# Kernel tuning notes

Measured on AMD Instinct MI355X. Metric: run time of the kernel, lower is better.

Reference implementation:

```python
import jax, jax.numpy as jnp
import numpy as np

N_NODES = 100000
N_EDGES = 1600000
FEAT = 128
HID = 128
CLASSES = 10
GRAPHS = 64


def gcn_conv(x, W, b, src, dst, n):
    # PyG GCNConv: h = x @ W; add self-loops; symmetric deg^{-1/2} norm; scatter-add; + bias
    h = x @ W
    src_f = jnp.concatenate([src, jnp.arange(n, dtype=src.dtype)])
    dst_f = jnp.concatenate([dst, jnp.arange(n, dtype=dst.dtype)])
    deg = jax.ops.segment_sum(jnp.ones_like(dst_f, dtype=h.dtype), dst_f, num_segments=n)
    dinv = jax.lax.rsqrt(jnp.where(deg > 0, deg, 1.0))
    norm = dinv[src_f] * dinv[dst_f]              # [E+N]
    msg = h[src_f] * norm[:, None]                # gather + scale
    out = jax.ops.segment_sum(msg, dst_f, num_segments=n)  # scatter-add
    return out + b


def global_mean_pool(x, batch, num_graphs):
    s = jax.ops.segment_sum(x, batch, num_segments=num_graphs)
    cnt = jax.ops.segment_sum(jnp.ones_like(batch, dtype=x.dtype), batch, num_segments=num_graphs)
    return s / jnp.maximum(cnt, 1.0)[:, None]


def setup_inputs() -> dict:
    key = jax.random.key(0)
    ks = jax.random.split(key, 10)
    x = jax.random.normal(ks[0], (N_NODES, FEAT), dtype=jnp.float32)
    edge_index = jax.random.randint(ks[1], (2, N_EDGES), 0, N_NODES, dtype=jnp.int64)
    batch = jnp.sort(jax.random.randint(ks[2], (N_NODES,), 0, GRAPHS, dtype=jnp.int64))
    def glorot(k, fi, fo):
        s = float(np.sqrt(6.0 / (fi + fo)))
        return jax.random.uniform(k, (fi, fo), jnp.float32, -s, s)
    return {
        "x": x, "edge_index": edge_index, "batch": batch,
        "W1": glorot(ks[3], FEAT, HID), "b1": jnp.zeros((HID,), jnp.float32),
        "W2": glorot(ks[4], HID, HID), "b2": jnp.zeros((HID,), jnp.float32),
        "W3": glorot(ks[5], HID, HID), "b3": jnp.zeros((HID,), jnp.float32),
        "Wlin": glorot(ks[6], HID, CLASSES), "blin": jnp.zeros((CLASSES,), jnp.float32),
    }


def reference(x, edge_index, batch, W1, b1, W2, b2, W3, b3, Wlin, blin):
    src, dst = edge_index[0], edge_index[1]
    n = x.shape[0]
    h = jax.nn.relu(gcn_conv(x, W1, b1, src, dst, n))
    h = jax.nn.relu(gcn_conv(h, W2, b2, src, dst, n))
    h = gcn_conv(h, W3, b3, src, dst, n)
    emb = global_mean_pool(h, batch, GRAPHS)      # [GRAPHS, HID]
    # dropout(p=0.5) is identity in eval mode
    logits = emb @ Wlin + blin                    # [GRAPHS, CLASSES]
    return logits, jnp.squeeze(emb)
```

## Files before the change

kernel.cpp:

```cpp
#include <hip/hip_runtime.h>
#include <hip/hip_bf16.h>
#include <stdint.h>

typedef unsigned int uint32;
typedef __attribute__((ext_vector_type(8))) short short8;
typedef __attribute__((ext_vector_type(4))) float float4v;

#define FEAT 128
#define NGRAPH 64
#define SBLK 256
#define STHR 256
#define SSEG 2
#define GB   256
#define NBK  512

__device__ __forceinline__ float bf2f_lo(uint32 v) {
    union { uint32 i; float f; } u; u.i = v << 16; return u.f;
}
__device__ __forceinline__ float bf2f_hi(uint32 v) {
    union { uint32 i; float f; } u; u.i = v & 0xffff0000u; return u.f;
}
__device__ __forceinline__ unsigned short f2bf(float f) {
    uint32 u = __builtin_bit_cast(uint32, f);
    uint32 r = (u + 0x7fffu + ((u >> 16) & 1u)) >> 16;
    return (unsigned short)r;
}
__device__ __forceinline__ uint32 f2bf2(float lo, float hi) {
    return (uint32)f2bf(lo) | ((uint32)f2bf(hi) << 16);
}

__global__ void k_bhist(const int* __restrict__ dst, int* __restrict__ bhist, int E) {
    __shared__ int h[NBK];
    int t = threadIdx.x, blk = blockIdx.x;
    for (int b = t; b < NBK; b += 256) h[b] = 0;
    __syncthreads();
    int chunk = (E + GB - 1) / GB;
    int lo = blk * chunk, hi = min(lo + chunk, E);
    for (int e = lo + t; e < hi; e += 256)
        atomicAdd(&h[dst[e] >> 8], 1);
    __syncthreads();
    for (int b = t; b < NBK; b += 256) bhist[blk * NBK + b] = h[b];
}

__global__ void k_boffs(int* __restrict__ bhist, int* __restrict__ bbase) {
    __shared__ int sc[NBK];
    int t = threadIdx.x;
    int tot = 0;
    for (int blk = 0; blk < GB; blk++) {
        int v = bhist[blk * NBK + t];
        bhist[blk * NBK + t] = tot;
        tot += v;
    }
    sc[t] = tot;
    __syncthreads();
    for (int off = 1; off < NBK; off <<= 1) {
        int v = (t >= off) ? sc[t - off] : 0;
        __syncthreads();
        sc[t] += v;
        __syncthreads();
    }
    bbase[t] = sc[t] - tot;
    if (t == NBK - 1) bbase[NBK] = sc[t];
}

__global__ void k_bscat(const int* __restrict__ src, const int* __restrict__ dst,
                        const int* __restrict__ bhist, const int* __restrict__ bbase,
                        uint32* __restrict__ ebuf, int E) {
    __shared__ int cur[NBK];
    int t = threadIdx.x, blk = blockIdx.x;
    for (int b = t; b < NBK; b += 256) cur[b] = bbase[b] + bhist[blk * NBK + b];
    __syncthreads();
    int chunk = (E + GB - 1) / GB;
    int lo = blk * chunk, hi = min(lo + chunk, E);
    for (int e = lo + t; e < hi; e += 256) {
        int d = dst[e], s = src[e];
        int b = d >> 8;
        int p = atomicAdd(&cur[b], 1);
        ebuf[p] = ((uint32)s << 8) | (uint32)(d & 255);
    }
}

__global__ void k_count2(const uint32* __restrict__ ebuf, const int* __restrict__ bbase,
                         int* __restrict__ counts, float* __restrict__ dinv, int N) {
    __shared__ int h[256];
    int t = threadIdx.x, b = blockIdx.x;
    h[t] = 0;
    __syncthreads();
    int e0 = bbase[b], e1 = bbase[b + 1];
    for (int e = e0 + t; e < e1; e += 256)
        atomicAdd(&h[ebuf[e] & 255u], 1);
    __syncthreads();
    int node = b * 256 + t;
    if (node < N) {
        counts[node] = h[t];
        dinv[node] = rsqrtf((float)h[t] + 1.0f);
    }
}

__global__ void k_fill2(const uint32* __restrict__ ebuf, const int* __restrict__ bbase,
                        const int* __restrict__ rowp, int* __restrict__ csrc, int N) {
    __shared__ int cur[256];
    int t = threadIdx.x, b = blockIdx.x;
    int node = b * 256 + t;
    cur[t] = (node < N) ? rowp[node] : 0;
    __syncthreads();
    int e0 = bbase[b], e1 = bbase[b + 1];
    for (int e = e0 + t; e < e1; e += 256) {
        uint32 v = ebuf[e];
        int p = atomicAdd(&cur[v & 255u], 1);
        csrc[p] = (int)(v >> 8);
    }
}

__global__ void k_scan_a(const int* __restrict__ counts, int* __restrict__ tbase,
                         int* __restrict__ bsum, int N) {
    __shared__ int sc[STHR];
    int t = threadIdx.x, b = blockIdx.x;
    int g = b * STHR + t;
    int lo = g * SSEG;
    int s = 0;
#pragma unroll
    for (int j = 0; j < SSEG; j++) {
        int i = lo + j;
        if (i < N) s += counts[i];
    }
    sc[t] = s;
    __syncthreads();
    for (int off = 1; off < STHR; off <<= 1) {
        int v = (t >= off) ? sc[t - off] : 0;
        __syncthreads();
        sc[t] += v;
        __syncthreads();
    }
    tbase[g] = sc[t] - s;
    if (t == STHR - 1) bsum[b] = sc[t];
}

__global__ void k_scan_b(const int* __restrict__ bsum, int* __restrict__ bbase2,
                         int* __restrict__ rowp, int N) {
    __shared__ int sc[SBLK];
    int t = threadIdx.x;
    int s = bsum[t];
    sc[t] = s;
    __syncthreads();
    for (int off = 1; off < SBLK; off <<= 1) {
        int v = (t >= off) ? sc[t - off] : 0;
        __syncthreads();
        sc[t] += v;
        __syncthreads();
    }
    bbase2[t] = sc[t] - s;
    if (t == SBLK - 1) rowp[N] = sc[t];
}

__global__ void k_scan_c(const int* __restrict__ counts, const int* __restrict__ tbase,
                         const int* __restrict__ bbase2, int* __restrict__ rowp, int N) {
    int t = threadIdx.x, b = blockIdx.x;
    int g = b * STHR + t;
    int base = bbase2[b] + tbase[g];
    int lo = g * SSEG;
#pragma unroll
    for (int j = 0; j < SSEG; j++) {
        int i = lo + j;
        if (i < N) { rowp[i] = base; base += counts[i]; }
    }
}

__global__ void k_wswz3(const float* __restrict__ W1, const float* __restrict__ W2,
                        const float* __restrict__ W3, unsigned short* __restrict__ o1,
                        unsigned short* __restrict__ o2, unsigned short* __restrict__ o3) {
    int wid = blockIdx.x >> 3;
    const float* W = (wid == 0) ? W1 : (wid == 1) ? W2 : W3;
    unsigned short* out = (wid == 0) ? o1 : (wid == 1) ? o2 : o3;
    int e = (blockIdx.x & 7) * 256 + threadIdx.x;
    int kt = e >> 9, ct = (e >> 6) & 7, lane = e & 63;
    int krow = kt * 32 + (lane >> 4) * 8;
    int col = ct * 16 + (lane & 15);
#pragma unroll
    for (int j = 0; j < 8; j++)
        out[e * 8 + j] = f2bf(W[(krow + j) * FEAT + col]);
}

template <bool F32IN>
__global__ void k_gemm(const void* __restrict__ Xp,
                       const unsigned short* __restrict__ Wswz,
                       const float* __restrict__ dinv,
                       unsigned short* __restrict__ Hb, int N) {
    __shared__ unsigned short Wl[FEAT * FEAT];
    {
        const uint4* Wg = (const uint4*)Wswz;
        uint4* Ws = (uint4*)Wl;
        for (int i = threadIdx.x; i < 2048; i += 256) Ws[i] = Wg[i];
    }
    __syncthreads();

    int wave = threadIdx.x >> 6, lane = threadIdx.x & 63;
    int r0 = (blockIdx.x * 4 + wave) * 16;
    if (r0 >= N) return;
    int m = lane & 15, q = lane >> 4;

    int arow = r0 + m; if (arow >= N) arow = N - 1;
    short8 a[4];
    if (F32IN) {
        const float* Ar = (const float*)Xp + (long)arow * FEAT;
#pragma unroll
        for (int kt = 0; kt < 4; kt++) {
            float4 u = *(const float4*)(Ar + kt * 32 + q * 8);
            float4 v = *(const float4*)(Ar + kt * 32 + q * 8 + 4);
            short8 t;
            t[0] = (short)f2bf(u.x); t[1] = (short)f2bf(u.y);
            t[2] = (short)f2bf(u.z); t[3] = (short)f2bf(u.w);
            t[4] = (short)f2bf(v.x); t[5] = (short)f2bf(v.y);
            t[6] = (short)f2bf(v.z); t[7] = (short)f2bf(v.w);
            a[kt] = t;
        }
    } else {
        const short8* Ar = (const short8*)((const unsigned short*)Xp + (long)arow * FEAT);
#pragma unroll
        for (int kt = 0; kt < 4; kt++) a[kt] = Ar[kt * 4 + q];
    }

    const short8* Bl = (const short8*)Wl;
    float4v acc[8];
#pragma unroll
    for (int ct = 0; ct < 8; ct++) acc[ct] = (float4v){0.f, 0.f, 0.f, 0.f};

#pragma unroll
    for (int ct = 0; ct < 8; ct++) {
        acc[ct] = __builtin_amdgcn_mfma_f32_16x16x32_bf16(a[0], Bl[(0 * 8 + ct) * 64 + lane], acc[ct], 0, 0, 0);
        acc[ct] = __builtin_amdgcn_mfma_f32_16x16x32_bf16(a[1], Bl[(1 * 8 + ct) * 64 + lane], acc[ct], 0, 0, 0);
        acc[ct] = __builtin_amdgcn_mfma_f32_16x16x32_bf16(a[2], Bl[(2 * 8 + ct) * 64 + lane], acc[ct], 0, 0, 0);
        acc[ct] = __builtin_amdgcn_mfma_f32_16x16x32_bf16(a[3], Bl[(3 * 8 + ct) * 64 + lane], acc[ct], 0, 0, 0);
    }

    float ds[4];
#pragma unroll
    for (int reg = 0; reg < 4; reg++) {
        int row = r0 + q * 4 + reg;
        ds[reg] = (row < N) ? dinv[row] : 0.f;
    }
#pragma unroll
    for (int ct = 0; ct < 8; ct++) {
#pragma unroll
        for (int reg = 0; reg < 4; reg++) {
            int row = r0 + q * 4 + reg;
            if (row < N) Hb[(long)row * FEAT + ct * 16 + m] = f2bf(acc[ct][reg] * ds[reg]);
        }
    }
}

__global__ void k_agg(const uint32* __restrict__ Hb,
                      const int* __restrict__ rowp, const int* __restrict__ csrc,
                      const float* __restrict__ dinv, const float* __restrict__ bias,
                      uint32* __restrict__ OUTb, int N, int relu) {
    int wave = threadIdx.x >> 6, lane = threadIdx.x & 63;
    int i = blockIdx.x * 4 + wave;
    if (i >= N) return;
    int f = lane & 31, half = lane >> 5;
    const uint2* H2 = (const uint2*)Hb;
    float a0 = 0.f, a1 = 0.f, a2 = 0.f, a3 = 0.f;
    int e0 = rowp[i], e1 = rowp[i + 1];
    int e = e0;
    for (; e + 16 <= e1; e += 16) {
        int  s[8];
        uint2 h[8];
#pragma unroll
        for (int j = 0; j < 8; j++) s[j] = csrc[e + 2 * j + half];
#pragma unroll
        for (int j = 0; j < 8; j++) h[j] = H2[(long)s[j] * 32 + f];
#pragma unroll
        for (int j = 0; j < 8; j++) {
            a0 += bf2f_lo(h[j].x); a1 += bf2f_hi(h[j].x);
            a2 += bf2f_lo(h[j].y); a3 += bf2f_hi(h[j].y);
        }
    }
    {
        int r = e1 - e;
        int  s[8];
        uint2 h[8];
#pragma unroll
        for (int j = 0; j < 8; j++) {
            int idx = 2 * j + half;
            if (idx < r) s[j] = csrc[e + idx];
        }
#pragma unroll
        for (int j = 0; j < 8; j++)
            if (2 * j + half < r) h[j] = H2[(long)s[j] * 32 + f];
#pragma unroll
        for (int j = 0; j < 8; j++)
            if (2 * j + half < r) {
                a0 += bf2f_lo(h[j].x); a1 += bf2f_hi(h[j].x);
                a2 += bf2f_lo(h[j].y); a3 += bf2f_hi(h[j].y);
            }
    }
    a0 += __shfl_xor(a0, 32);
    a1 += __shfl_xor(a1, 32);
    a2 += __shfl_xor(a2, 32);
    a3 += __shfl_xor(a3, 32);
    if (half == 0) {
        uint2 hv = H2[(long)i * 32 + f];
        a0 += bf2f_lo(hv.x); a1 += bf2f_hi(hv.x);
        a2 += bf2f_lo(hv.y); a3 += bf2f_hi(hv.y);
        float di = dinv[i];
        float4 bb = ((const float4*)bias)[f];
        a0 = a0 * di + bb.x; a1 = a1 * di + bb.y;
        a2 = a2 * di + bb.z; a3 = a3 * di + bb.w;
        if (relu) {
            a0 = fmaxf(a0, 0.f); a1 = fmaxf(a1, 0.f);
            a2 = fmaxf(a2, 0.f); a3 = fmaxf(a3, 0.f);
        }
        uint2 o;
        o.x = f2bf2(a0, a1);
        o.y = f2bf2(a2, a3);
        ((uint2*)OUTb)[(long)i * 32 + f] = o;
    }
}

__global__ void k_pool(const uint32* __restrict__ Gb, const int* __restrict__ batch,
                       float* __restrict__ pool, int* __restrict__ cntg, int N) {
    int t = threadIdx.x;
    int nb = gridDim.x;
    int chunk = (N + nb - 1) / nb;
    int lo = blockIdx.x * chunk, hi = min(lo + chunk, N);
    if (lo >= hi) return;
    float ax = 0.f, ay = 0.f;
    int cnt = 0;
    int cg = batch[lo];
    for (int i = lo; i < hi; i++) {
        int g = batch[i];
        if (g != cg) {
            atomicAdd(&pool[cg * FEAT + 2 * t], ax);
            atomicAdd(&pool[cg * FEAT + 2 * t + 1], ay);
            if (t == 0) atomicAdd(&cntg[cg], cnt);
            ax = ay = 0.f; cnt = 0; cg = g;
        }
        uint32 v = Gb[(long)i * 64 + t];
        ax += bf2f_lo(v); ay += bf2f_hi(v);
        cnt++;
    }
    atomicAdd(&pool[cg * FEAT + 2 * t], ax);
    atomicAdd(&pool[cg * FEAT + 2 * t + 1], ay);
    if (t == 0) atomicAdd(&cntg[cg], cnt);
}

__global__ void k_final(const float* __restrict__ pool, const int* __restrict__ cntg,
                        const float* __restrict__ Wlin, const float* __restrict__ blin,
                        float* __restrict__ out) {
    __shared__ float es[FEAT];
    int g = blockIdx.x, t = threadIdx.x;
    float c = (float)max(cntg[g], 1);
    float e = pool[g * FEAT + t] / c;
    es[t] = e;
    out[NGRAPH * 10 + g * FEAT + t] = e;
    __syncthreads();
    if (t < 10) {
        float a = blin[t];
        for (int k = 0; k < FEAT; k++)
            a += es[k] * Wlin[k * 10 + t];
        out[g * 10 + t] = a;
    }
}

extern "C" void kernel_launch(void* const* d_in, const int* in_sizes, int n_in,
                              void* d_out, int out_size, void* d_ws, size_t ws_size,
                              hipStream_t stream) {
    const float* x    = (const float*)d_in[0];
    const int*   ei   = (const int*)d_in[1];
    const int*   batch= (const int*)d_in[2];
    const float* W1   = (const float*)d_in[3];
    const float* b1   = (const float*)d_in[4];
    const float* W2   = (const float*)d_in[5];
    const float* b2   = (const float*)d_in[6];
    const float* W3   = (const float*)d_in[7];
    const float* b3   = (const float*)d_in[8];
    const float* Wlin = (const float*)d_in[9];
    const float* blin = (const float*)d_in[10];

    const int N = in_sizes[2];
    const int E = in_sizes[1] / 2;
    const int* src = ei;
    const int* dst = ei + E;
    const int NB = (N + 255) >> 8;

    char* w = (char*)d_ws;
    auto take = [&](size_t bytes) {
        char* p = w;
        w += (bytes + 255) & ~(size_t)255;
        return p;
    };
    int*    counts = (int*)   take((size_t)N * 4);
    float*  dinv   = (float*) take((size_t)N * 4);
    int*    rowp   = (int*)   take((size_t)(N + 1) * 4);
    int*    csrc   = (int*)   take((size_t)E * 4);
    uint32* ebuf   = (uint32*)take((size_t)E * 4);
    int*    bhist  = (int*)   take((size_t)GB * NBK * 4);
    int*    bbase  = (int*)   take((size_t)(NBK + 1) * 4);
    uint32* hbuf   = (uint32*)take((size_t)N * FEAT * 2);
    uint32* gbuf   = (uint32*)take((size_t)N * FEAT * 2);
    unsigned short* w1s = (unsigned short*)take(FEAT * FEAT * 2);
    unsigned short* w2s = (unsigned short*)take(FEAT * FEAT * 2);
    unsigned short* w3s = (unsigned short*)take(FEAT * FEAT * 2);
    float*  pool   = (float*) take((size_t)NGRAPH * FEAT * 4);
    int*    cntg   = (int*)   take((size_t)NGRAPH * 4);
    int*    tbase  = (int*)   take((size_t)SBLK * STHR * 4);
    int*    bsum   = (int*)   take((size_t)SBLK * 4);
    int*    bbase2 = (int*)   take((size_t)SBLK * 4);
    (void)ws_size; (void)n_in; (void)out_size;

    hipMemsetAsync(pool, 0, (size_t)NGRAPH * FEAT * 4, stream);
    hipMemsetAsync(cntg, 0, (size_t)NGRAPH * 4, stream);

    k_bhist <<<GB, 256, 0, stream>>>(dst, bhist, E);
    k_boffs <<<1, NBK, 0, stream>>>(bhist, bbase);
    k_bscat <<<GB, 256, 0, stream>>>(src, dst, bhist, bbase, ebuf, E);
    k_count2<<<NB, 256, 0, stream>>>(ebuf, bbase, counts, dinv, N);
    k_scan_a<<<SBLK, STHR, 0, stream>>>(counts, tbase, bsum, N);
    k_scan_b<<<1, SBLK, 0, stream>>>(bsum, bbase2, rowp, N);
    k_scan_c<<<SBLK, STHR, 0, stream>>>(counts, tbase, bbase2, rowp, N);
    k_fill2 <<<NB, 256, 0, stream>>>(ebuf, bbase, rowp, csrc, N);

    k_wswz3<<<24, 256, 0, stream>>>(W1, W2, W3, w1s, w2s, w3s);

    const int gemm_blocks = (N + 63) / 64;
    const int agg_blocks  = (N + 3) / 4;

    k_gemm<true> <<<gemm_blocks, 256, 0, stream>>>(x, w1s, dinv, (unsigned short*)hbuf, N);
    k_agg <<<agg_blocks, 256, 0, stream>>>(hbuf, rowp, csrc, dinv, b1, gbuf, N, 1);
    k_gemm<false><<<gemm_blocks, 256, 0, stream>>>(gbuf, w2s, dinv, (unsigned short*)hbuf, N);
    k_agg <<<agg_blocks, 256, 0, stream>>>(hbuf, rowp, csrc, dinv, b2, gbuf, N, 1);
    k_gemm<false><<<gemm_blocks, 256, 0, stream>>>(gbuf, w3s, dinv, (unsigned short*)hbuf, N);
    k_agg <<<agg_blocks, 256, 0, stream>>>(hbuf, rowp, csrc, dinv, b3, gbuf, N, 0);

    k_pool <<<1024, 64, 0, stream>>>(gbuf, batch, pool, cntg, N);
    k_final<<<NGRAPH, 128, 0, stream>>>(pool, cntg, Wlin, blin, (float*)d_out);
}
```

Before: 464.7 us.

## Fuse aggregation with next-layer GEMM and merge CSR count, scan and fill

New measurement: 637.5 us. 1.37x slower.

```diff
diff --git a/kernel.cpp b/kernel.cpp
--- a/kernel.cpp
+++ b/kernel.cpp
@@ -8,9 +8,6 @@
 
 #define FEAT 128
 #define NGRAPH 64
-#define SBLK 256
-#define STHR 256
-#define SSEG 2
 #define GB   256
 #define NBK  512
 
@@ -29,7 +26,7 @@
     return (uint32)f2bf(lo) | ((uint32)f2bf(hi) << 16);
 }
 
-__global__ void k_bhist(const int* __restrict__ dst, int* __restrict__ bhist, int E) {
+__global__ void k_bhist(const int* __restrict__ dst, int* __restrict__ bhistT, int E) {
     __shared__ int h[NBK];
     int t = threadIdx.x, blk = blockIdx.x;
     for (int b = t; b < NBK; b += 256) h[b] = 0;
@@ -39,16 +36,17 @@
     for (int e = lo + t; e < hi; e += 256)
         atomicAdd(&h[dst[e] >> 8], 1);
     __syncthreads();
-    for (int b = t; b < NBK; b += 256) bhist[blk * NBK + b] = h[b];
-}
-
-__global__ void k_boffs(int* __restrict__ bhist, int* __restrict__ bbase) {
+    for (int b = t; b < NBK; b += 256) bhistT[b * GB + blk] = h[b];
+}
+
+__global__ void k_boffs(int* __restrict__ bhistT, int* __restrict__ bbase) {
     __shared__ int sc[NBK];
     int t = threadIdx.x;
     int tot = 0;
+#pragma unroll 8
     for (int blk = 0; blk < GB; blk++) {
-        int v = bhist[blk * NBK + t];
-        bhist[blk * NBK + t] = tot;
+        int v = bhistT[t * GB + blk];
+        bhistT[t * GB + blk] = tot;
         tot += v;
     }
     sc[t] = tot;
@@ -64,11 +62,11 @@
 }
 
 __global__ void k_bscat(const int* __restrict__ src, const int* __restrict__ dst,
-                        const int* __restrict__ bhist, const int* __restrict__ bbase,
+                        const int* __restrict__ bhistT, const int* __restrict__ bbase,
                         uint32* __restrict__ ebuf, int E) {
     __shared__ int cur[NBK];
     int t = threadIdx.x, blk = blockIdx.x;
-    for (int b = t; b < NBK; b += 256) cur[b] = bbase[b] + bhist[blk * NBK + b];
+    for (int b = t; b < NBK; b += 256) cur[b] = bbase[b] + bhistT[b * GB + blk];
     __syncthreads();
     int chunk = (E + GB - 1) / GB;
     int lo = blk * chunk, hi = min(lo + chunk, E);
@@ -80,9 +78,11 @@
     }
 }
 
-__global__ void k_count2(const uint32* __restrict__ ebuf, const int* __restrict__ bbase,
-                         int* __restrict__ counts, float* __restrict__ dinv, int N) {
+__global__ void k_csr(const uint32* __restrict__ ebuf, const int* __restrict__ bbase,
+                      float* __restrict__ dinv, int* __restrict__ rowp,
+                      int* __restrict__ csrc, int N, int E) {
     __shared__ int h[256];
+    __shared__ int cur[256];
     int t = threadIdx.x, b = blockIdx.x;
     h[t] = 0;
     __syncthreads();
@@ -90,79 +90,28 @@
     for (int e = e0 + t; e < e1; e += 256)
         atomicAdd(&h[ebuf[e] & 255u], 1);
     __syncthreads();
+    int deg = h[t];
+    cur[t] = deg;
+    __syncthreads();
+    for (int off = 1; off < 256; off <<= 1) {
+        int v = (t >= off) ? cur[t - off] : 0;
+        __syncthreads();
+        cur[t] += v;
+        __syncthreads();
+    }
+    int r = bbase[b] + cur[t] - deg;
     int node = b * 256 + t;
     if (node < N) {
-        counts[node] = h[t];
-        dinv[node] = rsqrtf((float)h[t] + 1.0f);
-    }
-}
-
-__global__ void k_fill2(const uint32* __restrict__ ebuf, const int* __restrict__ bbase,
-                        const int* __restrict__ rowp, int* __restrict__ csrc, int N) {
-    __shared__ int cur[256];
-    int t = threadIdx.x, b = blockIdx.x;
-    int node = b * 256 + t;
-    cur[t] = (node < N) ? rowp[node] : 0;
-    __syncthreads();
-    int e0 = bbase[b], e1 = bbase[b + 1];
+        rowp[node] = r;
+        dinv[node] = rsqrtf((float)deg + 1.0f);
+    }
+    if (b == 0 && t == 0) rowp[N] = E;
+    cur[t] = r;
+    __syncthreads();
     for (int e = e0 + t; e < e1; e += 256) {
         uint32 v = ebuf[e];
         int p = atomicAdd(&cur[v & 255u], 1);
         csrc[p] = (int)(v >> 8);
-    }
-}
-
-__global__ void k_scan_a(const int* __restrict__ counts, int* __restrict__ tbase,
-                         int* __restrict__ bsum, int N) {
-    __shared__ int sc[STHR];
-    int t = threadIdx.x, b = blockIdx.x;
-    int g = b * STHR + t;
-    int lo = g * SSEG;
-    int s = 0;
-#pragma unroll
-    for (int j = 0; j < SSEG; j++) {
-        int i = lo + j;
-        if (i < N) s += counts[i];
-    }
-    sc[t] = s;
-    __syncthreads();
-    for (int off = 1; off < STHR; off <<= 1) {
-        int v = (t >= off) ? sc[t - off] : 0;
-        __syncthreads();
-        sc[t] += v;
-        __syncthreads();
-    }
-    tbase[g] = sc[t] - s;
-    if (t == STHR - 1) bsum[b] = sc[t];
-}
-
-__global__ void k_scan_b(const int* __restrict__ bsum, int* __restrict__ bbase2,
-                         int* __restrict__ rowp, int N) {
-    __shared__ int sc[SBLK];
-    int t = threadIdx.x;
-    int s = bsum[t];
-    sc[t] = s;
-    __syncthreads();
-    for (int off = 1; off < SBLK; off <<= 1) {
-        int v = (t >= off) ? sc[t - off] : 0;
-        __syncthreads();
-        sc[t] += v;
-        __syncthreads();
-    }
-    bbase2[t] = sc[t] - s;
-    if (t == SBLK - 1) rowp[N] = sc[t];
-}
-
-__global__ void k_scan_c(const int* __restrict__ counts, const int* __restrict__ tbase,
-                         const int* __restrict__ bbase2, int* __restrict__ rowp, int N) {
-    int t = threadIdx.x, b = blockIdx.x;
-    int g = b * STHR + t;
-    int base = bbase2[b] + tbase[g];
-    int lo = g * SSEG;
-#pragma unroll
-    for (int j = 0; j < SSEG; j++) {
-        int i = lo + j;
-        if (i < N) { rowp[i] = base; base += counts[i]; }
     }
 }
 
@@ -181,11 +130,10 @@
         out[e * 8 + j] = f2bf(W[(krow + j) * FEAT + col]);
 }
 
-template <bool F32IN>
-__global__ void k_gemm(const void* __restrict__ Xp,
-                       const unsigned short* __restrict__ Wswz,
-                       const float* __restrict__ dinv,
-                       unsigned short* __restrict__ Hb, int N) {
+__global__ void k_gemm1(const float* __restrict__ Xp,
+                        const unsigned short* __restrict__ Wswz,
+                        const float* __restrict__ dinv,
+                        unsigned short* __restrict__ Hb, int N) {
     __shared__ unsigned short Wl[FEAT * FEAT];
     {
         const uint4* Wg = (const uint4*)Wswz;
@@ -201,30 +149,25 @@
 
     int arow = r0 + m; if (arow >= N) arow = N - 1;
     short8 a[4];
-    if (F32IN) {
-        const float* Ar = (const float*)Xp + (long)arow * FEAT;
+    {
+        const float* Ar = Xp + (long)arow * FEAT;
 #pragma unroll
         for (int kt = 0; kt < 4; kt++) {
             float4 u = *(const float4*)(Ar + kt * 32 + q * 8);
             float4 v = *(const float4*)(Ar + kt * 32 + q * 8 + 4);
-            short8 t;
-            t[0] = (short)f2bf(u.x); t[1] = (short)f2bf(u.y);
-            t[2] = (short)f2bf(u.z); t[3] = (short)f2bf(u.w);
-            t[4] = (short)f2bf(v.x); t[5] = (short)f2bf(v.y);
-            t[6] = (short)f2bf(v.z); t[7] = (short)f2bf(v.w);
-            a[kt] = t;
-        }
-    } else {
-        const short8* Ar = (const short8*)((const unsigned short*)Xp + (long)arow * FEAT);
-#pragma unroll
-        for (int kt = 0; kt < 4; kt++) a[kt] = Ar[kt * 4 + q];
+            short8 tv;
+            tv[0] = (short)f2bf(u.x); tv[1] = (short)f2bf(u.y);
+            tv[2] = (short)f2bf(u.z); tv[3] = (short)f2bf(u.w);
+            tv[4] = (short)f2bf(v.x); tv[5] = (short)f2bf(v.y);
+            tv[6] = (short)f2bf(v.z); tv[7] = (short)f2bf(v.w);
+            a[kt] = tv;
+        }
     }
 
     const short8* Bl = (const short8*)Wl;
     float4v acc[8];
 #pragma unroll
     for (int ct = 0; ct < 8; ct++) acc[ct] = (float4v){0.f, 0.f, 0.f, 0.f};
-
 #pragma unroll
     for (int ct = 0; ct < 8; ct++) {
         acc[ct] = __builtin_amdgcn_mfma_f32_16x16x32_bf16(a[0], Bl[(0 * 8 + ct) * 64 + lane], acc[ct], 0, 0, 0);
@@ -249,10 +192,125 @@
     }
 }
 
+__global__ void k_fuse(const uint32* __restrict__ Hin,
+                       const int* __restrict__ rowp, const int* __restrict__ csrc,
+                       const float* __restrict__ dinv, const float* __restrict__ bias,
+                       const unsigned short* __restrict__ Wswz,
+                       unsigned short* __restrict__ Hout, int N) {
+    __shared__ unsigned short Wl[FEAT * FEAT];
+    __shared__ unsigned short At[4][16 * FEAT];
+    {
+        const uint4* Wg = (const uint4*)Wswz;
+        uint4* Ws = (uint4*)Wl;
+        for (int i = threadIdx.x; i < 2048; i += 256) Ws[i] = Wg[i];
+    }
+    int wave = threadIdx.x >> 6, lane = threadIdx.x & 63;
+    int f = lane & 31, half = lane >> 5;
+    const uint2* H2 = (const uint2*)Hin;
+    int base = blockIdx.x * 64 + wave * 16;
+
+    for (int n = 0; n < 16; n++) {
+        int i = base + n;
+        if (i < N) {
+            float a0 = 0.f, a1 = 0.f, a2 = 0.f, a3 = 0.f;
+            int e0 = rowp[i], e1 = rowp[i + 1];
+            int e = e0;
+            for (; e + 16 <= e1; e += 16) {
+                int  s[8];
+                uint2 h[8];
+#pragma unroll
+                for (int j = 0; j < 8; j++) s[j] = csrc[e + 2 * j + half];
+#pragma unroll
+                for (int j = 0; j < 8; j++) h[j] = H2[(long)s[j] * 32 + f];
+#pragma unroll
+                for (int j = 0; j < 8; j++) {
+                    a0 += bf2f_lo(h[j].x); a1 += bf2f_hi(h[j].x);
+                    a2 += bf2f_lo(h[j].y); a3 += bf2f_hi(h[j].y);
+                }
+            }
+            {
+                int r = e1 - e;
+                int  s[8];
+                uint2 h[8];
+#pragma unroll
+                for (int j = 0; j < 8; j++) {
+                    int idx = 2 * j + half;
+                    if (idx < r) s[j] = csrc[e + idx];
+                }
+#pragma unroll
+                for (int j = 0; j < 8; j++)
+                    if (2 * j + half < r) h[j] = H2[(long)s[j] * 32 + f];
+#pragma unroll
+                for (int j = 0; j < 8; j++)
+                    if (2 * j + half < r) {
+                        a0 += bf2f_lo(h[j].x); a1 += bf2f_hi(h[j].x);
+                        a2 += bf2f_lo(h[j].y); a3 += bf2f_hi(h[j].y);
+                    }
+            }
+            a0 += __shfl_xor(a0, 32);
+            a1 += __shfl_xor(a1, 32);
+            a2 += __shfl_xor(a2, 32);
+            a3 += __shfl_xor(a3, 32);
+            if (half == 0) {
+                uint2 hv = H2[(long)i * 32 + f];
+                a0 += bf2f_lo(hv.x); a1 += bf2f_hi(hv.x);
+                a2 += bf2f_lo(hv.y); a3 += bf2f_hi(hv.y);
+                float di = dinv[i];
+                float4 bb = ((const float4*)bias)[f];
+                a0 = fmaxf(a0 * di + bb.x, 0.f);
+                a1 = fmaxf(a1 * di + bb.y, 0.f);
+                a2 = fmaxf(a2 * di + bb.z, 0.f);
+                a3 = fmaxf(a3 * di + bb.w, 0.f);
+                uint2 o;
+                o.x = f2bf2(a0, a1);
+                o.y = f2bf2(a2, a3);
+                ((uint2*)&At[wave][n * FEAT])[f] = o;
+            }
+        } else if (half == 0) {
+            uint2 z; z.x = 0; z.y = 0;
+            ((uint2*)&At[wave][n * FEAT])[f] = z;
+        }
+    }
+    __syncthreads();
+
+    int m = lane & 15, q = lane >> 4;
+    short8 a[4];
+    {
+        const short8* Ar = (const short8*)&At[wave][m * FEAT];
+#pragma unroll
+        for (int kt = 0; kt < 4; kt++) a[kt] = Ar[kt * 4 + q];
+    }
+    const short8* Bl = (const short8*)Wl;
+    float4v acc[8];
+#pragma unroll
+    for (int ct = 0; ct < 8; ct++) acc[ct] = (float4v){0.f, 0.f, 0.f, 0.f};
+#pragma unroll
+    for (int ct = 0; ct < 8; ct++) {
+        acc[ct] = __builtin_amdgcn_mfma_f32_16x16x32_bf16(a[0], Bl[(0 * 8 + ct) * 64 + lane], acc[ct], 0, 0, 0);
+        acc[ct] = __builtin_amdgcn_mfma_f32_16x16x32_bf16(a[1], Bl[(1 * 8 + ct) * 64 + lane], acc[ct], 0, 0, 0);
+        acc[ct] = __builtin_amdgcn_mfma_f32_16x16x32_bf16(a[2], Bl[(2 * 8 + ct) * 64 + lane], acc[ct], 0, 0, 0);
+        acc[ct] = __builtin_amdgcn_mfma_f32_16x16x32_bf16(a[3], Bl[(3 * 8 + ct) * 64 + lane], acc[ct], 0, 0, 0);
+    }
+    float ds[4];
+#pragma unroll
+    for (int reg = 0; reg < 4; reg++) {
+        int row = base + q * 4 + reg;
+        ds[reg] = (row < N) ? dinv[row] : 0.f;
+    }
+#pragma unroll
+    for (int ct = 0; ct < 8; ct++) {
+#pragma unroll
+        for (int reg = 0; reg < 4; reg++) {
+            int row = base + q * 4 + reg;
+            if (row < N) Hout[(long)row * FEAT + ct * 16 + m] = f2bf(acc[ct][reg] * ds[reg]);
+        }
+    }
+}
+
 __global__ void k_agg(const uint32* __restrict__ Hb,
                       const int* __restrict__ rowp, const int* __restrict__ csrc,
                       const float* __restrict__ dinv, const float* __restrict__ bias,
-                      uint32* __restrict__ OUTb, int N, int relu) {
+                      uint32* __restrict__ OUTb, int N) {
     int wave = threadIdx.x >> 6, lane = threadIdx.x & 63;
     int i = blockIdx.x * 4 + wave;
     if (i >= N) return;
@@ -305,10 +363,6 @@
         float4 bb = ((const float4*)bias)[f];
         a0 = a0 * di + bb.x; a1 = a1 * di + bb.y;
         a2 = a2 * di + bb.z; a3 = a3 * di + bb.w;
-        if (relu) {
-            a0 = fmaxf(a0, 0.f); a1 = fmaxf(a1, 0.f);
-            a2 = fmaxf(a2, 0.f); a3 = fmaxf(a3, 0.f);
-        }
         uint2 o;
         o.x = f2bf2(a0, a1);
         o.y = f2bf2(a2, a3);
@@ -388,48 +442,41 @@
         w += (bytes + 255) & ~(size_t)255;
         return p;
     };
-    int*    counts = (int*)   take((size_t)N * 4);
     float*  dinv   = (float*) take((size_t)N * 4);
     int*    rowp   = (int*)   take((size_t)(N + 1) * 4);
     int*    csrc   = (int*)   take((size_t)E * 4);
     uint32* ebuf   = (uint32*)take((size_t)E * 4);
-    int*    bhist  = (int*)   take((size_t)GB * NBK * 4);
+    int*    bhistT = (int*)   take((size_t)GB * NBK * 4);
     int*    bbase  = (int*)   take((size_t)(NBK + 1) * 4);
-    uint32* hbuf   = (uint32*)take((size_t)N * FEAT * 2);
+    uint32* h1     = (uint32*)take((size_t)N * FEAT * 2);
+    uint32* h2     = (uint32*)take((size_t)N * FEAT * 2);
     uint32* gbuf   = (uint32*)take((size_t)N * FEAT * 2);
     unsigned short* w1s = (unsigned short*)take(FEAT * FEAT * 2);
     unsigned short* w2s = (unsigned short*)take(FEAT * FEAT * 2);
     unsigned short* w3s = (unsigned short*)take(FEAT * FEAT * 2);
     float*  pool   = (float*) take((size_t)NGRAPH * FEAT * 4);
     int*    cntg   = (int*)   take((size_t)NGRAPH * 4);
-    int*    tbase  = (int*)   take((size_t)SBLK * STHR * 4);
-    int*    bsum   = (int*)   take((size_t)SBLK * 4);
-    int*    bbase2 = (int*)   take((size_t)SBLK * 4);
     (void)ws_size; (void)n_in; (void)out_size;
 
     hipMemsetAsync(pool, 0, (size_t)NGRAPH * FEAT * 4, stream);
     hipMemsetAsync(cntg, 0, (size_t)NGRAPH * 4, stream);
 
-    k_bhist <<<GB, 256, 0, stream>>>(dst, bhist, E);
-    k_boffs <<<1, NBK, 0, stream>>>(bhist, bbase);
-    k_bscat <<<GB, 256, 0, stream>>>(src, dst, bhist, bbase, ebuf, E);
-    k_count2<<<NB, 256, 0, stream>>>(ebuf, bbase, counts, dinv, N);
-    k_scan_a<<<SBLK, STHR, 0, stream>>>(counts, tbase, bsum, N);
-    k_scan_b<<<1, SBLK, 0, stream>>>(bsum, bbase2, rowp, N);
-    k_scan_c<<<SBLK, STHR, 0, stream>>>(counts, tbase, bbase2, rowp, N);
-    k_fill2 <<<NB, 256, 0, stream>>>(ebuf, bbase, rowp, csrc, N);
+    k_bhist<<<GB, 256, 0, stream>>>(dst, bhistT, E);
+    k_boffs<<<1, NBK, 0, stream>>>(bhistT, bbase);
+    k_bscat<<<GB, 256, 0, stream>>>(src, dst, bhistT, bbase, ebuf, E);
+    k_csr  <<<NB, 256, 0, stream>>>(ebuf, bbase, dinv, rowp, csrc, N, E);
 
     k_wswz3<<<24, 256, 0, stream>>>(W1, W2, W3, w1s, w2s, w3s);
 
-    const int gemm_blocks = (N + 63) / 64;
+    const int tile_blocks = (N + 63) / 64;
     const int agg_blocks  = (N + 3) / 4;
 
-    k_gemm<true> <<<gemm_blocks, 256, 0, stream>>>(x, w1s, dinv, (unsigned short*)hbuf, N);
-    k_agg <<<agg_blocks, 256, 0, stream>>>(hbuf, rowp, csrc, dinv, b1, gbuf, N, 1);
-    k_gemm<false><<<gemm_blocks, 256, 0, stream>>>(gbuf, w2s, dinv, (unsigned short*)hbuf, N);
-    k_agg <<<agg_blocks, 256, 0, stream>>>(hbuf, rowp, csrc, dinv, b2, gbuf, N, 1);
-    k_gemm<false><<<gemm_blocks, 256, 0, stream>>>(gbuf, w3s, dinv, (unsigned short*)hbuf, N);
-    k_agg <<<agg_blocks, 256, 0, stream>>>(hbuf, rowp, csrc, dinv, b3, gbuf, N, 0);
+    k_gemm1<<<tile_blocks, 256, 0, stream>>>(x, w1s, dinv, (unsigned short*)h1, N);
+    k_fuse<<<tile_blocks, 256, 0, stream>>>(h1, rowp, csrc, dinv, b1, w2s,
+                                            (unsigned short*)h2, N);
+    k_fuse<<<tile_blocks, 256, 0, stream>>>(h2, rowp, csrc, dinv, b2, w3s,
+                                            (unsigned short*)h1, N);
+    k_agg<<<agg_blocks, 256, 0, stream>>>(h1, rowp, csrc, dinv, b3, gbuf, N);
 
     k_pool <<<1024, 64, 0, stream>>>(gbuf, batch, pool, cntg, N);
     k_final<<<NGRAPH, 128, 0, stream>>>(pool, cntg, Wlin, blin, (float*)d_out);
```

## Fuse CSR count, scan and fill into one kernel; transpose bucket histogram

Applied to the files above, without the earlier changes.

Measured after the change: 483.7 us. 1.04x slower.

```diff
diff --git a/kernel.cpp b/kernel.cpp
--- a/kernel.cpp
+++ b/kernel.cpp
@@ -8,9 +8,6 @@
 
 #define FEAT 128
 #define NGRAPH 64
-#define SBLK 256
-#define STHR 256
-#define SSEG 2
 #define GB   256
 #define NBK  512
 
@@ -29,7 +26,7 @@
     return (uint32)f2bf(lo) | ((uint32)f2bf(hi) << 16);
 }
 
-__global__ void k_bhist(const int* __restrict__ dst, int* __restrict__ bhist, int E) {
+__global__ void k_bhist(const int* __restrict__ dst, int* __restrict__ bhistT, int E) {
     __shared__ int h[NBK];
     int t = threadIdx.x, blk = blockIdx.x;
     for (int b = t; b < NBK; b += 256) h[b] = 0;
@@ -39,16 +36,17 @@
     for (int e = lo + t; e < hi; e += 256)
         atomicAdd(&h[dst[e] >> 8], 1);
     __syncthreads();
-    for (int b = t; b < NBK; b += 256) bhist[blk * NBK + b] = h[b];
-}
-
-__global__ void k_boffs(int* __restrict__ bhist, int* __restrict__ bbase) {
+    for (int b = t; b < NBK; b += 256) bhistT[b * GB + blk] = h[b];
+}
+
+__global__ void k_boffs(int* __restrict__ bhistT, int* __restrict__ bbase) {
     __shared__ int sc[NBK];
     int t = threadIdx.x;
     int tot = 0;
+#pragma unroll 8
     for (int blk = 0; blk < GB; blk++) {
-        int v = bhist[blk * NBK + t];
-        bhist[blk * NBK + t] = tot;
+        int v = bhistT[t * GB + blk];
+        bhistT[t * GB + blk] = tot;
         tot += v;
     }
     sc[t] = tot;
@@ -64,11 +62,11 @@
 }
 
 __global__ void k_bscat(const int* __restrict__ src, const int* __restrict__ dst,
-                        const int* __restrict__ bhist, const int* __restrict__ bbase,
+                        const int* __restrict__ bhistT, const int* __restrict__ bbase,
                         uint32* __restrict__ ebuf, int E) {
     __shared__ int cur[NBK];
     int t = threadIdx.x, blk = blockIdx.x;
-    for (int b = t; b < NBK; b += 256) cur[b] = bbase[b] + bhist[blk * NBK + b];
+    for (int b = t; b < NBK; b += 256) cur[b] = bbase[b] + bhistT[b * GB + blk];
     __syncthreads();
     int chunk = (E + GB - 1) / GB;
     int lo = blk * chunk, hi = min(lo + chunk, E);
@@ -80,9 +78,11 @@
     }
 }
 
-__global__ void k_count2(const uint32* __restrict__ ebuf, const int* __restrict__ bbase,
-                         int* __restrict__ counts, float* __restrict__ dinv, int N) {
+__global__ void k_csr(const uint32* __restrict__ ebuf, const int* __restrict__ bbase,
+                      float* __restrict__ dinv, int* __restrict__ rowp,
+                      int* __restrict__ csrc, int N, int E) {
     __shared__ int h[256];
+    __shared__ int cur[256];
     int t = threadIdx.x, b = blockIdx.x;
     h[t] = 0;
     __syncthreads();
@@ -90,79 +90,28 @@
     for (int e = e0 + t; e < e1; e += 256)
         atomicAdd(&h[ebuf[e] & 255u], 1);
     __syncthreads();
+    int deg = h[t];
+    cur[t] = deg;
+    __syncthreads();
+    for (int off = 1; off < 256; off <<= 1) {
+        int v = (t >= off) ? cur[t - off] : 0;
+        __syncthreads();
+        cur[t] += v;
+        __syncthreads();
+    }
+    int r = bbase[b] + cur[t] - deg;
     int node = b * 256 + t;
     if (node < N) {
-        counts[node] = h[t];
-        dinv[node] = rsqrtf((float)h[t] + 1.0f);
-    }
-}
-
-__global__ void k_fill2(const uint32* __restrict__ ebuf, const int* __restrict__ bbase,
-                        const int* __restrict__ rowp, int* __restrict__ csrc, int N) {
-    __shared__ int cur[256];
-    int t = threadIdx.x, b = blockIdx.x;
-    int node = b * 256 + t;
-    cur[t] = (node < N) ? rowp[node] : 0;
-    __syncthreads();
-    int e0 = bbase[b], e1 = bbase[b + 1];
+        rowp[node] = r;
+        dinv[node] = rsqrtf((float)deg + 1.0f);
+    }
+    if (b == 0 && t == 0) rowp[N] = E;
+    cur[t] = r;
+    __syncthreads();
     for (int e = e0 + t; e < e1; e += 256) {
         uint32 v = ebuf[e];
         int p = atomicAdd(&cur[v & 255u], 1);
         csrc[p] = (int)(v >> 8);
-    }
-}
-
-__global__ void k_scan_a(const int* __restrict__ counts, int* __restrict__ tbase,
-                         int* __restrict__ bsum, int N) {
-    __shared__ int sc[STHR];
-    int t = threadIdx.x, b = blockIdx.x;
-    int g = b * STHR + t;
-    int lo = g * SSEG;
-    int s = 0;
-#pragma unroll
-    for (int j = 0; j < SSEG; j++) {
-        int i = lo + j;
-        if (i < N) s += counts[i];
-    }
-    sc[t] = s;
-    __syncthreads();
-    for (int off = 1; off < STHR; off <<= 1) {
-        int v = (t >= off) ? sc[t - off] : 0;
-        __syncthreads();
-        sc[t] += v;
-        __syncthreads();
-    }
-    tbase[g] = sc[t] - s;
-    if (t == STHR - 1) bsum[b] = sc[t];
-}
-
-__global__ void k_scan_b(const int* __restrict__ bsum, int* __restrict__ bbase2,
-                         int* __restrict__ rowp, int N) {
-    __shared__ int sc[SBLK];
-    int t = threadIdx.x;
-    int s = bsum[t];
-    sc[t] = s;
-    __syncthreads();
-    for (int off = 1; off < SBLK; off <<= 1) {
-        int v = (t >= off) ? sc[t - off] : 0;
-        __syncthreads();
-        sc[t] += v;
-        __syncthreads();
-    }
-    bbase2[t] = sc[t] - s;
-    if (t == SBLK - 1) rowp[N] = sc[t];
-}
-
-__global__ void k_scan_c(const int* __restrict__ counts, const int* __restrict__ tbase,
-                         const int* __restrict__ bbase2, int* __restrict__ rowp, int N) {
-    int t = threadIdx.x, b = blockIdx.x;
-    int g = b * STHR + t;
-    int base = bbase2[b] + tbase[g];
-    int lo = g * SSEG;
-#pragma unroll
-    for (int j = 0; j < SSEG; j++) {
-        int i = lo + j;
-        if (i < N) { rowp[i] = base; base += counts[i]; }
     }
 }
 
@@ -207,12 +156,12 @@
         for (int kt = 0; kt < 4; kt++) {
             float4 u = *(const float4*)(Ar + kt * 32 + q * 8);
             float4 v = *(const float4*)(Ar + kt * 32 + q * 8 + 4);
-            short8 t;
-            t[0] = (short)f2bf(u.x); t[1] = (short)f2bf(u.y);
-            t[2] = (short)f2bf(u.z); t[3] = (short)f2bf(u.w);
-            t[4] = (short)f2bf(v.x); t[5] = (short)f2bf(v.y);
-            t[6] = (short)f2bf(v.z); t[7] = (short)f2bf(v.w);
-            a[kt] = t;
+            short8 tv;
+            tv[0] = (short)f2bf(u.x); tv[1] = (short)f2bf(u.y);
+            tv[2] = (short)f2bf(u.z); tv[3] = (short)f2bf(u.w);
+            tv[4] = (short)f2bf(v.x); tv[5] = (short)f2bf(v.y);
+            tv[6] = (short)f2bf(v.z); tv[7] = (short)f2bf(v.w);
+            a[kt] = tv;
         }
     } else {
         const short8* Ar = (const short8*)((const unsigned short*)Xp + (long)arow * FEAT);
@@ -224,7 +173,6 @@
     float4v acc[8];
 #pragma unroll
     for (int ct = 0; ct < 8; ct++) acc[ct] = (float4v){0.f, 0.f, 0.f, 0.f};
-
 #pragma unroll
     for (int ct = 0; ct < 8; ct++) {
         acc[ct] = __builtin_amdgcn_mfma_f32_16x16x32_bf16(a[0], Bl[(0 * 8 + ct) * 64 + lane], acc[ct], 0, 0, 0);
@@ -388,12 +336,11 @@
         w += (bytes + 255) & ~(size_t)255;
         return p;
     };
-    int*    counts = (int*)   take((size_t)N * 4);
     float*  dinv   = (float*) take((size_t)N * 4);
     int*    rowp   = (int*)   take((size_t)(N + 1) * 4);
     int*    csrc   = (int*)   take((size_t)E * 4);
     uint32* ebuf   = (uint32*)take((size_t)E * 4);
-    int*    bhist  = (int*)   take((size_t)GB * NBK * 4);
+    int*    bhistT = (int*)   take((size_t)GB * NBK * 4);
     int*    bbase  = (int*)   take((size_t)(NBK + 1) * 4);
     uint32* hbuf   = (uint32*)take((size_t)N * FEAT * 2);
     uint32* gbuf   = (uint32*)take((size_t)N * FEAT * 2);
@@ -402,34 +349,27 @@
     unsigned short* w3s = (unsigned short*)take(FEAT * FEAT * 2);
     float*  pool   = (float*) take((size_t)NGRAPH * FEAT * 4);
     int*    cntg   = (int*)   take((size_t)NGRAPH * 4);
-    int*    tbase  = (int*)   take((size_t)SBLK * STHR * 4);
-    int*    bsum   = (int*)   take((size_t)SBLK * 4);
-    int*    bbase2 = (int*)   take((size_t)SBLK * 4);
     (void)ws_size; (void)n_in; (void)out_size;
 
     hipMemsetAsync(pool, 0, (size_t)NGRAPH * FEAT * 4, stream);
     hipMemsetAsync(cntg, 0, (size_t)NGRAPH * 4, stream);
 
-    k_bhist <<<GB, 256, 0, stream>>>(dst, bhist, E);
-    k_boffs <<<1, NBK, 0, stream>>>(bhist, bbase);
-    k_bscat <<<GB, 256, 0, stream>>>(src, dst, bhist, bbase, ebuf, E);
-    k_count2<<<NB, 256, 0, stream>>>(ebuf, bbase, counts, dinv, N);
-    k_scan_a<<<SBLK, STHR, 0, stream>>>(counts, tbase, bsum, N);
-    k_scan_b<<<1, SBLK, 0, stream>>>(bsum, bbase2, rowp, N);
-    k_scan_c<<<SBLK, STHR, 0, stream>>>(counts, tbase, bbase2, rowp, N);
-    k_fill2 <<<NB, 256, 0, stream>>>(ebuf, bbase, rowp, csrc, N);
+    k_bhist<<<GB, 256, 0, stream>>>(dst, bhistT, E);
+    k_boffs<<<1, NBK, 0, stream>>>(bhistT, bbase);
+    k_bscat<<<GB, 256, 0, stream>>>(src, dst, bhistT, bbase, ebuf, E);
+    k_csr  <<<NB, 256, 0, stream>>>(ebuf, bbase, dinv, rowp, csrc, N, E);
 
     k_wswz3<<<24, 256, 0, stream>>>(W1, W2, W3, w1s, w2s, w3s);
 
-    const int gemm_blocks = (N + 63) / 64;
+    const int tile_blocks = (N + 63) / 64;
     const int agg_blocks  = (N + 3) / 4;
 
-    k_gemm<true> <<<gemm_blocks, 256, 0, stream>>>(x, w1s, dinv, (unsigned short*)hbuf, N);
-    k_agg <<<agg_blocks, 256, 0, stream>>>(hbuf, rowp, csrc, dinv, b1, gbuf, N, 1);
-    k_gemm<false><<<gemm_blocks, 256, 0, stream>>>(gbuf, w2s, dinv, (unsigned short*)hbuf, N);
-    k_agg <<<agg_blocks, 256, 0, stream>>>(hbuf, rowp, csrc, dinv, b2, gbuf, N, 1);
-    k_gemm<false><<<gemm_blocks, 256, 0, stream>>>(gbuf, w3s, dinv, (unsigned short*)hbuf, N);
-    k_agg <<<agg_blocks, 256, 0, stream>>>(hbuf, rowp, csrc, dinv, b3, gbuf, N, 0);
+    k_gemm<true> <<<tile_blocks, 256, 0, stream>>>(x, w1s, dinv, (unsigned short*)hbuf, N);
+    k_agg<<<agg_blocks, 256, 0, stream>>>(hbuf, rowp, csrc, dinv, b1, gbuf, N, 1);
+    k_gemm<false><<<tile_blocks, 256, 0, stream>>>(gbuf, w2s, dinv, (unsigned short*)hbuf, N);
+    k_agg<<<agg_blocks, 256, 0, stream>>>(hbuf, rowp, csrc, dinv, b2, gbuf, N, 1);
+    k_gemm<false><<<tile_blocks, 256, 0, stream>>>(gbuf, w3s, dinv, (unsigned short*)hbuf, N);
+    k_agg<<<agg_blocks, 256, 0, stream>>>(hbuf, rowp, csrc, dinv, b3, gbuf, N, 0);
 
     k_pool <<<1024, 64, 0, stream>>>(gbuf, batch, pool, cntg, N);
     k_final<<<NGRAPH, 128, 0, stream>>>(pool, cntg, Wlin, blin, (float*)d_out);
```
